# Kernel optimization log

Measured on AMD Instinct MI355X. Metric: run time of the kernel, lower is better.

Reference implementation:

```python
import jax, jax.numpy as jnp
import numpy as np

F = 26          # field_size
D = 16          # embed_dim
B = 16384       # batch
VOCABS = [1000] * F
OFFSETS = np.concatenate([[0], np.cumsum(VOCABS)[:-1]]).astype(np.int32)
IU, JU = np.triu_indices(F, k=1)   # 325 pairs (i<j)
P = IU.shape[0]
BN_EPS = 1e-3   # Keras BatchNormalization default epsilon


def setup_inputs() -> dict:
    key = jax.random.key(0)
    ks = jax.random.split(key, 8)
    s = 0.05  # keras 'random_normal' initializer stddev
    return {
        "x": jax.random.randint(ks[0], (B, F), 0, 1000, dtype=jnp.int32),
        "emb_table": jax.random.normal(ks[1], (sum(VOCABS) + 1, D), jnp.float32) * s,
        "se_w1": jax.random.normal(ks[2], (F, F // 2), jnp.float32) * s,
        "se_w2": jax.random.normal(ks[3], (F // 2, F), jnp.float32) * s,
        "bl_w": jax.random.normal(ks[4], (P, D, D), jnp.float32) * s,
        "w1": jax.random.normal(ks[5], (F * (F - 1) * D, 64), jnp.float32) * s,
        "b1": jnp.zeros((64,), jnp.float32),
        "g1": jnp.ones((64,), jnp.float32),
        "be1": jnp.zeros((64,), jnp.float32),
        "m1": jnp.zeros((64,), jnp.float32),
        "v1": jnp.ones((64,), jnp.float32),
        "w2": jax.random.normal(ks[6], (64, 32), jnp.float32) * s,
        "b2": jnp.zeros((32,), jnp.float32),
        "g2": jnp.ones((32,), jnp.float32),
        "be2": jnp.zeros((32,), jnp.float32),
        "m2": jnp.zeros((32,), jnp.float32),
        "v2": jnp.ones((32,), jnp.float32),
        "w3": jax.random.normal(ks[7], (32, 1), jnp.float32) * s,
        "b3": jnp.zeros((1,), jnp.float32),
    }


def _bilinear(v, bl_w):
    # v: [B, F, D]; shared W stack over the 325 ordered pairs (i<j)
    # tmp[p] = (v_i @ W_p) * v_j  -> [B, P, D]
    return jnp.einsum('bpd,pde->bpe', v[:, IU], bl_w) * v[:, JU]


def _bn(h, g, b, m, v):
    return g * (h - m) * jax.lax.rsqrt(v + BN_EPS) + b


def reference(x, emb_table, se_w1, se_w2, bl_w,
              w1, b1, g1, be1, m1, v1,
              w2, b2, g2, be2, m2, v2,
              w3, b3):
    ids = x + jnp.asarray(OFFSETS)
    e = emb_table[ids]                         # [B, F, D]
    # SE layer: mean-pool over embed dim, two ReLU dense layers, rescale
    z = e.mean(axis=-1)                        # [B, F]
    A = jax.nn.relu(jax.nn.relu(z @ se_w1) @ se_w2)
    se = e * A[..., None]                      # [B, F, D]
    # Bilinear interaction (same weights for both calls)
    p = _bilinear(e, bl_w).reshape(e.shape[0], -1)     # [B, P*D]
    se_p = _bilinear(se, bl_w).reshape(e.shape[0], -1)
    h = jnp.concatenate([p, se_p], axis=-1)    # [B, F*(F-1)*D]
    # MLP with inference-mode BatchNorm; dropout=0 is a no-op
    h = jax.nn.relu(_bn(h @ w1 + b1, g1, be1, m1, v1))
    h = jax.nn.relu(_bn(h @ w2 + b2, g2, be2, m2, v2))
    return jax.nn.sigmoid(h @ w3 + b3)         # [B, 1]
```

## Files before the change

### kernel.cpp

```cpp
#include <hip/hip_runtime.h>
#include <cstdint>
#include <cstddef>


#define F_FIELDS 26
#define P_PAIRS 325
#define PAD_PAIRS 336
#define BATCH 16384
#define BN_EPS 1e-3f

typedef short bf16x8 __attribute__((ext_vector_type(8)));
typedef float f32x4 __attribute__((ext_vector_type(4)));

struct PairTab { unsigned char iu[PAD_PAIRS]; unsigned char ju[PAD_PAIRS]; };
static constexpr PairTab make_pairs() {
    PairTab t{};
    int p = 0;
    for (int a = 0; a < F_FIELDS; ++a)
        for (int b = a + 1; b < F_FIELDS; ++b) { t.iu[p] = (unsigned char)a; t.ju[p] = (unsigned char)b; ++p; }
    for (; p < PAD_PAIRS; ++p) { t.iu[p] = 0; t.ju[p] = 0; }
    return t;
}
__constant__ PairTab PT = make_pairs();

__device__ __forceinline__ unsigned short bf16u(float v) {
    unsigned u = __float_as_uint(v);
    unsigned r = (u + 0x7fffu + ((u >> 16) & 1u)) >> 16;
    return (unsigned short)r;
}
__device__ __forceinline__ unsigned pk_bf16(float lo, float hi) {
    return (unsigned)bf16u(lo) | ((unsigned)bf16u(hi) << 16);
}
__device__ __forceinline__ float bflo(unsigned d) { return __uint_as_float(d << 16); }
__device__ __forceinline__ float bfhi(unsigned d) { return __uint_as_float(d & 0xffff0000u); }
__device__ __forceinline__ unsigned pk_trunc(float u, float cu) {
    return __builtin_amdgcn_perm(__float_as_uint(cu), __float_as_uint(u), 0x07060302u);
}

__global__ __launch_bounds__(256) void k_wprep(const float* __restrict__ w1,
        const float* __restrict__ blw, unsigned short* __restrict__ w1catL,
        unsigned short* __restrict__ wcatL) {
    const int p = blockIdx.x;
    const int tid = threadIdx.x;
    if (p >= P_PAIRS) {
        int4 z = make_int4(0, 0, 0, 0);
        *(int4*)(w1catL + (size_t)p * 2048 + tid * 8) = z;
        if (tid < 64) *(int4*)(wcatL + (size_t)p * 512 + tid * 8) = z;
        return;
    }
    __shared__ float wu[1024], wv[1024], wb[256];
    ((float4*)wu)[tid] = ((const float4*)(w1 + (size_t)p * 1024))[tid];
    ((float4*)wv)[tid] = ((const float4*)(w1 + 332800 + (size_t)p * 1024))[tid];
    if (tid < 64) ((float4*)wb)[tid] = ((const float4*)(blw + (size_t)p * 256))[tid];
    __syncthreads();
    {
        int nt = tid >> 6, lane = tid & 63, ln = lane & 15, q = lane >> 4;
        int o = nt * 16 + ln;
        unsigned short outv[8];
        #pragma unroll
        for (int j = 0; j < 8; ++j) {
            int k = q * 8 + j, d = k >> 1, su = k & 1;
            outv[j] = bf16u(su ? wv[d * 64 + o] : wu[d * 64 + o]);
        }
        *(int4*)(w1catL + (size_t)p * 2048 + tid * 8) = *(const int4*)outv;
    }
    if (tid < 64) {
        int ln = tid & 15, q = tid >> 4;
        unsigned short outv[8];
        #pragma unroll
        for (int j = 0; j < 8; ++j) {
            int din = q * 8 + j;
            outv[j] = (din < 16) ? bf16u(wb[din * 16 + ln]) : (unsigned short)0;
        }
        *(int4*)(wcatL + (size_t)p * 512 + tid * 8) = *(const int4*)outv;
    }
}

union __align__(16) SMem {
    struct {
        unsigned short eS[32 * 424];
        float aS[F_FIELDS * 32];
    } a;
    struct {
        unsigned ysh[8 * 4 * 64 * 4];
        float h1s[32 * 65];
        float h2s[32 * 36];
    } b;
};

__global__ __launch_bounds__(512, 4) void k_main(const int* __restrict__ x,
        const float* __restrict__ emb, const float* __restrict__ sw1,
        const float* __restrict__ sw2, const unsigned short* __restrict__ w1catL,
        const unsigned short* __restrict__ wcatL,
        const float* __restrict__ b1, const float* __restrict__ g1,
        const float* __restrict__ be1, const float* __restrict__ m1,
        const float* __restrict__ v1,
        const float* __restrict__ w2, const float* __restrict__ b2,
        const float* __restrict__ g2, const float* __restrict__ be2,
        const float* __restrict__ m2, const float* __restrict__ v2,
        const float* __restrict__ w3, const float* __restrict__ b3,
        float* __restrict__ out) {
    __shared__ SMem sm;
    __shared__ float z_s[32][F_FIELDS];
    __shared__ float sw1_s[F_FIELDS * 13];
    __shared__ float sw2_s[13 * F_FIELDS];
    const int tid = threadIdx.x;
    const int b0 = blockIdx.x * 32;
    unsigned short* eS = sm.a.eS;
    float* aS = sm.a.aS;

    for (int i = tid; i < F_FIELDS * 13; i += 512) { sw1_s[i] = sw1[i]; sw2_s[i] = sw2[i]; }
    for (int idx = tid; idx < 32 * F_FIELDS; idx += 512) {
        int r = idx / F_FIELDS, f = idx - r * F_FIELDS;
        int id = x[(b0 + r) * F_FIELDS + f] + f * 1000;
        const float4* src = (const float4*)(emb + (size_t)id * 16);
        float4 v0 = src[0], v1l = src[1], v2l = src[2], v3l = src[3];
        int4 o0, o1;
        o0.x = (int)pk_bf16(v0.x, v0.y);  o0.y = (int)pk_bf16(v0.z, v0.w);
        o0.z = (int)pk_bf16(v1l.x, v1l.y); o0.w = (int)pk_bf16(v1l.z, v1l.w);
        o1.x = (int)pk_bf16(v2l.x, v2l.y); o1.y = (int)pk_bf16(v2l.z, v2l.w);
        o1.z = (int)pk_bf16(v3l.x, v3l.y); o1.w = (int)pk_bf16(v3l.z, v3l.w);
        *(int4*)(eS + r * 424 + f * 16) = o0;
        *(int4*)(eS + r * 424 + f * 16 + 8) = o1;
        float s = v0.x + v0.y + v0.z + v0.w + v1l.x + v1l.y + v1l.z + v1l.w
                + v2l.x + v2l.y + v2l.z + v2l.w + v3l.x + v3l.y + v3l.z + v3l.w;
        z_s[r][f] = s * (1.0f / 16.0f);
    }
    __syncthreads();
    if (tid < 32) {
        float s1[13];
        #pragma unroll
        for (int o = 0; o < 13; ++o) {
            float acc0 = 0.f;
            #pragma unroll
            for (int f = 0; f < F_FIELDS; ++f) acc0 = fmaf(z_s[tid][f], sw1_s[f * 13 + o], acc0);
            s1[o] = fmaxf(acc0, 0.0f);
        }
        #pragma unroll
        for (int f = 0; f < F_FIELDS; ++f) {
            float acc0 = 0.f;
            #pragma unroll
            for (int o = 0; o < 13; ++o) acc0 = fmaf(s1[o], sw2_s[o * F_FIELDS + f], acc0);
            aS[f * 32 + tid] = fmaxf(acc0, 0.0f);
        }
    }
    __syncthreads();

    const int w    = tid >> 6;
    const int lane = tid & 63;
    const int ln   = lane & 15;
    const int q    = lane >> 4;
    const int p0 = w * 42, p1 = p0 + 42;

    f32x4 acc[2][4];
    #pragma unroll
    for (int a = 0; a < 2; ++a)
        #pragma unroll
        for (int b = 0; b < 4; ++b) acc[a][b] = (f32x4){0.f, 0.f, 0.f, 0.f};
    const f32x4 zero4 = {0.f, 0.f, 0.f, 0.f};

    bf16x8 wa[2];
    bf16x8 wb[2][4];
    #pragma unroll
    for (int s = 0; s < 2; ++s) {
        int pp = p0 + s;
        wa[s] = __builtin_bit_cast(bf16x8, *(const int4*)(wcatL + (size_t)pp * 512 + lane * 8));
        #pragma unroll
        for (int nt = 0; nt < 4; ++nt)
            wb[s][nt] = __builtin_bit_cast(bf16x8, *(const int4*)(w1catL + (size_t)pp * 2048 + nt * 512 + lane * 8));
    }

    int iu_c = PT.iu[p0];
    bf16x8 eiB[2];
    float ai[2];
    #pragma unroll
    for (int mt = 0; mt < 2; ++mt) {
        eiB[mt] = __builtin_bit_cast(bf16x8,
            *(const int4*)(eS + (mt * 16 + ln) * 424 + iu_c * 16 + (q & 1) * 8));
        ai[mt] = aS[iu_c * 32 + mt * 16 + ln];
    }

    #pragma unroll 2
    for (int p = p0; p < p1; ++p) {
        const int slot = (p - p0) & 1;
        const int ju = PT.ju[p];
        uint2 ejv[2];
        float cv[2];
        #pragma unroll
        for (int mt = 0; mt < 2; ++mt) {
            ejv[mt] = *(const uint2*)(eS + (mt * 16 + ln) * 424 + ju * 16 + q * 4);
            cv[mt]  = ai[mt] * aS[ju * 32 + mt * 16 + ln];
        }
        #pragma unroll
        for (int mt = 0; mt < 2; ++mt) {
            f32x4 t = __builtin_amdgcn_mfma_f32_16x16x32_bf16(wa[slot], eiB[mt], zero4, 0, 0, 0);
            float e0 = bflo(ejv[mt].x), e1 = bfhi(ejv[mt].x);
            float e2 = bflo(ejv[mt].y), e3 = bfhi(ejv[mt].y);
            float c  = cv[mt];
            float u0 = t[0] * e0, u1 = t[1] * e1, u2 = t[2] * e2, u3 = t[3] * e3;
            int4 af;
            af.x = (int)pk_trunc(u0, c * u0);
            af.y = (int)pk_trunc(u1, c * u1);
            af.z = (int)pk_trunc(u2, c * u2);
            af.w = (int)pk_trunc(u3, c * u3);
            bf16x8 A = __builtin_bit_cast(bf16x8, af);
            #pragma unroll
            for (int nt = 0; nt < 4; ++nt)
                acc[mt][nt] = __builtin_amdgcn_mfma_f32_16x16x32_bf16(A, wb[slot][nt], acc[mt][nt], 0, 0, 0);
        }
        {
            const int pf = (p + 2 < p1) ? (p + 2) : (p1 - 1);
            wa[slot] = __builtin_bit_cast(bf16x8, *(const int4*)(wcatL + (size_t)pf * 512 + lane * 8));
            #pragma unroll
            for (int nt = 0; nt < 4; ++nt)
                wb[slot][nt] = __builtin_bit_cast(bf16x8, *(const int4*)(w1catL + (size_t)pf * 2048 + nt * 512 + lane * 8));
        }
        const int pn = (p + 1 < p1) ? (p + 1) : p;
        const int iu_n = PT.iu[pn];
        if (iu_n != iu_c) {
            iu_c = iu_n;
            #pragma unroll
            for (int mt = 0; mt < 2; ++mt) {
                eiB[mt] = __builtin_bit_cast(bf16x8,
                    *(const int4*)(eS + (mt * 16 + ln) * 424 + iu_c * 16 + (q & 1) * 8));
                ai[mt] = aS[iu_c * 32 + mt * 16 + ln];
            }
        }
    }

    __syncthreads();
    unsigned* ysh = sm.b.ysh;
    float* h1s = sm.b.h1s;
    float* h2s = sm.b.h2s;
    #pragma unroll
    for (int mt = 0; mt < 2; ++mt)
        #pragma unroll
        for (int nh = 0; nh < 2; ++nh) {
            int nt0 = nh * 2, nt1 = nh * 2 + 1;
            int4 v;
            v.x = (int)pk_bf16(acc[mt][nt0][0], acc[mt][nt0][1]);
            v.y = (int)pk_bf16(acc[mt][nt0][2], acc[mt][nt0][3]);
            v.z = (int)pk_bf16(acc[mt][nt1][0], acc[mt][nt1][1]);
            v.w = (int)pk_bf16(acc[mt][nt1][2], acc[mt][nt1][3]);
            *(int4*)(ysh + ((w * 4 + mt * 2 + nh) * 64 + lane) * 4) = v;
        }
    __syncthreads();

    if (tid < 256) {
        const int s = tid >> 6, lane2 = tid & 63, ln2 = lane2 & 15, q2 = lane2 >> 4;
        const int mt = s >> 1, nh = s & 1;
        const int c0 = nh * 32 + ln2, c1 = c0 + 16;
        const float sc0 = g1[c0] * rsqrtf(v1[c0] + BN_EPS);
        const float of0 = be1[c0] + sc0 * (b1[c0] - m1[c0]);
        const float sc1 = g1[c1] * rsqrtf(v1[c1] + BN_EPS);
        const float of1 = be1[c1] + sc1 * (b1[c1] - m1[c1]);
        float s8[8];
        #pragma unroll
        for (int i = 0; i < 8; ++i) s8[i] = 0.f;
        #pragma unroll
        for (int wv = 0; wv < 8; ++wv) {
            int4 v = *(const int4*)(ysh + ((wv * 4 + s) * 64 + lane2) * 4);
            s8[0] += bflo((unsigned)v.x); s8[1] += bfhi((unsigned)v.x);
            s8[2] += bflo((unsigned)v.y); s8[3] += bfhi((unsigned)v.y);
            s8[4] += bflo((unsigned)v.z); s8[5] += bfhi((unsigned)v.z);
            s8[6] += bflo((unsigned)v.w); s8[7] += bfhi((unsigned)v.w);
        }
        const int row0 = mt * 16 + q2 * 4;
        #pragma unroll
        for (int r = 0; r < 4; ++r) {
            h1s[(row0 + r) * 65 + c0] = fmaxf(s8[r] * sc0 + of0, 0.f);
            h1s[(row0 + r) * 65 + c1] = fmaxf(s8[4 + r] * sc1 + of1, 0.f);
        }
    }
    __syncthreads();

    {
        const int row = tid >> 4, gg = tid & 15;
        const int o0 = gg * 2, o1 = o0 + 1;
        float a0 = 0.f, a1 = 0.f;
        #pragma unroll 8
        for (int k = 0; k < 64; ++k) {
            float hk = h1s[row * 65 + k];
            float2 wv = *(const float2*)(w2 + k * 32 + o0);
            a0 = fmaf(hk, wv.x, a0);
            a1 = fmaf(hk, wv.y, a1);
        }
        float val0 = g2[o0] * (a0 + b2[o0] - m2[o0]) * rsqrtf(v2[o0] + BN_EPS) + be2[o0];
        float val1 = g2[o1] * (a1 + b2[o1] - m2[o1]) * rsqrtf(v2[o1] + BN_EPS) + be2[o1];
        h2s[row * 36 + o0] = fmaxf(val0, 0.f);
        h2s[row * 36 + o1] = fmaxf(val1, 0.f);
    }
    __syncthreads();
    if (tid < 32) {
        float sacc = b3[0];
        #pragma unroll
        for (int k = 0; k < 32; ++k) sacc = fmaf(h2s[tid * 36 + k], w3[k], sacc);
        out[b0 + tid] = 1.0f / (1.0f + expf(-sacc));
    }
}

extern "C" void kernel_launch(void* const* d_in, const int* in_sizes, int n_in,
                              void* d_out, int out_size, void* d_ws, size_t ws_size,
                              hipStream_t stream) {
    const int*   x   = (const int*)d_in[0];
    const float* emb = (const float*)d_in[1];
    const float* sw1 = (const float*)d_in[2];
    const float* sw2 = (const float*)d_in[3];
    const float* blw = (const float*)d_in[4];
    const float* w1  = (const float*)d_in[5];
    const float* b1  = (const float*)d_in[6];
    const float* g1  = (const float*)d_in[7];
    const float* be1 = (const float*)d_in[8];
    const float* m1  = (const float*)d_in[9];
    const float* v1  = (const float*)d_in[10];
    const float* w2  = (const float*)d_in[11];
    const float* b2  = (const float*)d_in[12];
    const float* g2  = (const float*)d_in[13];
    const float* be2 = (const float*)d_in[14];
    const float* m2  = (const float*)d_in[15];
    const float* v2  = (const float*)d_in[16];
    const float* w3  = (const float*)d_in[17];
    const float* b3  = (const float*)d_in[18];
    float* out = (float*)d_out;

    char* ws = (char*)d_ws;
    unsigned short* w1catL = (unsigned short*)ws;
    unsigned short* wcatL  = (unsigned short*)(ws + 1376256);

    hipLaunchKernelGGL(k_wprep, dim3(PAD_PAIRS), dim3(256), 0, stream, w1, blw, w1catL, wcatL);
    hipLaunchKernelGGL(k_main,  dim3(512), dim3(512), 0, stream,
                       x, emb, sw1, sw2, w1catL, wcatL,
                       b1, g1, be1, m1, v1, w2, b2, g2, be2, m2, v2, w3, b3, out);
}
```

Before: 148.4 us.

## Double batch tile to 64 rows with 1024-thread blocks splitting output columns

Each block now processes 64 batch rows with 16 waves. Pairs of waves share a pair-range and split the 64 output columns, so each wave loads half the W1 fragments but reuses them over four row tiles. The goal is to halve per-row global weight traffic, at the cost of twice-recomputed first-stage bilinear MFMAs per wave pair. The first-layer reduction now runs in two passes over shared memory with extra barriers. The SE mean is recomputed from the bf16 shared copy instead of fp32 sums, which slightly changes precision. The grid drops to 256 blocks, so fewer workgroups are spread across the CUs.

```diff
diff --git a/kernel.cpp b/kernel.cpp
--- a/kernel.cpp
+++ b/kernel.cpp
@@ -78,17 +78,17 @@
 
 union __align__(16) SMem {
     struct {
-        unsigned short eS[32 * 424];
-        float aS[F_FIELDS * 32];
+        unsigned short eS[64 * 424];
+        float aS[F_FIELDS * 64];
     } a;
     struct {
         unsigned ysh[8 * 4 * 64 * 4];
-        float h1s[32 * 65];
-        float h2s[32 * 36];
+        float h1s[64 * 65];
+        float h2s[64 * 36];
     } b;
 };
 
-__global__ __launch_bounds__(512, 4) void k_main(const int* __restrict__ x,
+__global__ __launch_bounds__(1024, 4) void k_main(const int* __restrict__ x,
         const float* __restrict__ emb, const float* __restrict__ sw1,
         const float* __restrict__ sw2, const unsigned short* __restrict__ w1catL,
         const unsigned short* __restrict__ wcatL,
@@ -101,16 +101,15 @@
         const float* __restrict__ w3, const float* __restrict__ b3,
         float* __restrict__ out) {
     __shared__ SMem sm;
-    __shared__ float z_s[32][F_FIELDS];
     __shared__ float sw1_s[F_FIELDS * 13];
     __shared__ float sw2_s[13 * F_FIELDS];
     const int tid = threadIdx.x;
-    const int b0 = blockIdx.x * 32;
+    const int b0 = blockIdx.x * 64;
     unsigned short* eS = sm.a.eS;
     float* aS = sm.a.aS;
 
-    for (int i = tid; i < F_FIELDS * 13; i += 512) { sw1_s[i] = sw1[i]; sw2_s[i] = sw2[i]; }
-    for (int idx = tid; idx < 32 * F_FIELDS; idx += 512) {
+    for (int i = tid; i < F_FIELDS * 13; i += 1024) { sw1_s[i] = sw1[i]; sw2_s[i] = sw2[i]; }
+    for (int idx = tid; idx < 64 * F_FIELDS; idx += 1024) {
         int r = idx / F_FIELDS, f = idx - r * F_FIELDS;
         int id = x[(b0 + r) * F_FIELDS + f] + f * 1000;
         const float4* src = (const float4*)(emb + (size_t)id * 16);
@@ -122,18 +121,30 @@
         o1.z = (int)pk_bf16(v3l.x, v3l.y); o1.w = (int)pk_bf16(v3l.z, v3l.w);
         *(int4*)(eS + r * 424 + f * 16) = o0;
         *(int4*)(eS + r * 424 + f * 16 + 8) = o1;
-        float s = v0.x + v0.y + v0.z + v0.w + v1l.x + v1l.y + v1l.z + v1l.w
-                + v2l.x + v2l.y + v2l.z + v2l.w + v3l.x + v3l.y + v3l.z + v3l.w;
-        z_s[r][f] = s * (1.0f / 16.0f);
-    }
-    __syncthreads();
-    if (tid < 32) {
+    }
+    __syncthreads();
+    if (tid < 64) {
+        float z[F_FIELDS];
+        #pragma unroll
+        for (int f = 0; f < F_FIELDS; ++f) {
+            const int4* e16 = (const int4*)(eS + tid * 424 + f * 16);
+            int4 va = e16[0], vb = e16[1];
+            float s = bflo((unsigned)va.x) + bfhi((unsigned)va.x)
+                    + bflo((unsigned)va.y) + bfhi((unsigned)va.y)
+                    + bflo((unsigned)va.z) + bfhi((unsigned)va.z)
+                    + bflo((unsigned)va.w) + bfhi((unsigned)va.w)
+                    + bflo((unsigned)vb.x) + bfhi((unsigned)vb.x)
+                    + bflo((unsigned)vb.y) + bfhi((unsigned)vb.y)
+                    + bflo((unsigned)vb.z) + bfhi((unsigned)vb.z)
+                    + bflo((unsigned)vb.w) + bfhi((unsigned)vb.w);
+            z[f] = s * (1.0f / 16.0f);
+        }
         float s1[13];
         #pragma unroll
         for (int o = 0; o < 13; ++o) {
             float acc0 = 0.f;
             #pragma unroll
-            for (int f = 0; f < F_FIELDS; ++f) acc0 = fmaf(z_s[tid][f], sw1_s[f * 13 + o], acc0);
+            for (int f = 0; f < F_FIELDS; ++f) acc0 = fmaf(z[f], sw1_s[f * 13 + o], acc0);
             s1[o] = fmaxf(acc0, 0.0f);
         }
         #pragma unroll
@@ -141,7 +152,7 @@
             float acc0 = 0.f;
             #pragma unroll
             for (int o = 0; o < 13; ++o) acc0 = fmaf(s1[o], sw2_s[o * F_FIELDS + f], acc0);
-            aS[f * 32 + tid] = fmaxf(acc0, 0.0f);
+            aS[f * 64 + tid] = fmaxf(acc0, 0.0f);
         }
     }
     __syncthreads();
@@ -150,80 +161,83 @@
     const int lane = tid & 63;
     const int ln   = lane & 15;
     const int q    = lane >> 4;
-    const int p0 = w * 42, p1 = p0 + 42;
-
-    f32x4 acc[2][4];
+    const int c    = w >> 1;
+    const int nh   = w & 1;
+    const int p0 = c * 42, p1 = p0 + 42;
+
+    f32x4 acc[4][2];
     #pragma unroll
-    for (int a = 0; a < 2; ++a)
-        #pragma unroll
-        for (int b = 0; b < 4; ++b) acc[a][b] = (f32x4){0.f, 0.f, 0.f, 0.f};
+    for (int a = 0; a < 4; ++a)
+        #pragma unroll
+        for (int b = 0; b < 2; ++b) acc[a][b] = (f32x4){0.f, 0.f, 0.f, 0.f};
     const f32x4 zero4 = {0.f, 0.f, 0.f, 0.f};
 
     bf16x8 wa[2];
-    bf16x8 wb[2][4];
+    bf16x8 wb[2][2];
     #pragma unroll
     for (int s = 0; s < 2; ++s) {
         int pp = p0 + s;
         wa[s] = __builtin_bit_cast(bf16x8, *(const int4*)(wcatL + (size_t)pp * 512 + lane * 8));
         #pragma unroll
-        for (int nt = 0; nt < 4; ++nt)
-            wb[s][nt] = __builtin_bit_cast(bf16x8, *(const int4*)(w1catL + (size_t)pp * 2048 + nt * 512 + lane * 8));
+        for (int ntl = 0; ntl < 2; ++ntl)
+            wb[s][ntl] = __builtin_bit_cast(bf16x8,
+                *(const int4*)(w1catL + (size_t)pp * 2048 + (nh * 2 + ntl) * 512 + lane * 8));
     }
 
     int iu_c = PT.iu[p0];
-    bf16x8 eiB[2];
-    float ai[2];
+    bf16x8 eiB[4];
+    float ai[4];
     #pragma unroll
-    for (int mt = 0; mt < 2; ++mt) {
+    for (int mt = 0; mt < 4; ++mt) {
         eiB[mt] = __builtin_bit_cast(bf16x8,
             *(const int4*)(eS + (mt * 16 + ln) * 424 + iu_c * 16 + (q & 1) * 8));
-        ai[mt] = aS[iu_c * 32 + mt * 16 + ln];
+        ai[mt] = aS[iu_c * 64 + mt * 16 + ln];
     }
 
     #pragma unroll 2
     for (int p = p0; p < p1; ++p) {
         const int slot = (p - p0) & 1;
         const int ju = PT.ju[p];
-        uint2 ejv[2];
-        float cv[2];
-        #pragma unroll
-        for (int mt = 0; mt < 2; ++mt) {
+        uint2 ejv[4];
+        float cv[4];
+        #pragma unroll
+        for (int mt = 0; mt < 4; ++mt) {
             ejv[mt] = *(const uint2*)(eS + (mt * 16 + ln) * 424 + ju * 16 + q * 4);
-            cv[mt]  = ai[mt] * aS[ju * 32 + mt * 16 + ln];
-        }
-        #pragma unroll
-        for (int mt = 0; mt < 2; ++mt) {
+            cv[mt]  = ai[mt] * aS[ju * 64 + mt * 16 + ln];
+        }
+        #pragma unroll
+        for (int mt = 0; mt < 4; ++mt) {
             f32x4 t = __builtin_amdgcn_mfma_f32_16x16x32_bf16(wa[slot], eiB[mt], zero4, 0, 0, 0);
             float e0 = bflo(ejv[mt].x), e1 = bfhi(ejv[mt].x);
             float e2 = bflo(ejv[mt].y), e3 = bfhi(ejv[mt].y);
-            float c  = cv[mt];
+            float cc = cv[mt];
             float u0 = t[0] * e0, u1 = t[1] * e1, u2 = t[2] * e2, u3 = t[3] * e3;
             int4 af;
-            af.x = (int)pk_trunc(u0, c * u0);
-            af.y = (int)pk_trunc(u1, c * u1);
-            af.z = (int)pk_trunc(u2, c * u2);
-            af.w = (int)pk_trunc(u3, c * u3);
+            af.x = (int)pk_trunc(u0, cc * u0);
+            af.y = (int)pk_trunc(u1, cc * u1);
+            af.z = (int)pk_trunc(u2, cc * u2);
+            af.w = (int)pk_trunc(u3, cc * u3);
             bf16x8 A = __builtin_bit_cast(bf16x8, af);
-            #pragma unroll
-            for (int nt = 0; nt < 4; ++nt)
-                acc[mt][nt] = __builtin_amdgcn_mfma_f32_16x16x32_bf16(A, wb[slot][nt], acc[mt][nt], 0, 0, 0);
+            acc[mt][0] = __builtin_amdgcn_mfma_f32_16x16x32_bf16(A, wb[slot][0], acc[mt][0], 0, 0, 0);
+            acc[mt][1] = __builtin_amdgcn_mfma_f32_16x16x32_bf16(A, wb[slot][1], acc[mt][1], 0, 0, 0);
         }
         {
             const int pf = (p + 2 < p1) ? (p + 2) : (p1 - 1);
             wa[slot] = __builtin_bit_cast(bf16x8, *(const int4*)(wcatL + (size_t)pf * 512 + lane * 8));
             #pragma unroll
-            for (int nt = 0; nt < 4; ++nt)
-                wb[slot][nt] = __builtin_bit_cast(bf16x8, *(const int4*)(w1catL + (size_t)pf * 2048 + nt * 512 + lane * 8));
+            for (int ntl = 0; ntl < 2; ++ntl)
+                wb[slot][ntl] = __builtin_bit_cast(bf16x8,
+                    *(const int4*)(w1catL + (size_t)pf * 2048 + (nh * 2 + ntl) * 512 + lane * 8));
         }
         const int pn = (p + 1 < p1) ? (p + 1) : p;
         const int iu_n = PT.iu[pn];
         if (iu_n != iu_c) {
             iu_c = iu_n;
             #pragma unroll
-            for (int mt = 0; mt < 2; ++mt) {
+            for (int mt = 0; mt < 4; ++mt) {
                 eiB[mt] = __builtin_bit_cast(bf16x8,
                     *(const int4*)(eS + (mt * 16 + ln) * 424 + iu_c * 16 + (q & 1) * 8));
-                ai[mt] = aS[iu_c * 32 + mt * 16 + ln];
+                ai[mt] = aS[iu_c * 64 + mt * 16 + ln];
             }
         }
     }
@@ -232,47 +246,48 @@
     unsigned* ysh = sm.b.ysh;
     float* h1s = sm.b.h1s;
     float* h2s = sm.b.h2s;
+
     #pragma unroll
-    for (int mt = 0; mt < 2; ++mt)
-        #pragma unroll
-        for (int nh = 0; nh < 2; ++nh) {
-            int nt0 = nh * 2, nt1 = nh * 2 + 1;
-            int4 v;
-            v.x = (int)pk_bf16(acc[mt][nt0][0], acc[mt][nt0][1]);
-            v.y = (int)pk_bf16(acc[mt][nt0][2], acc[mt][nt0][3]);
-            v.z = (int)pk_bf16(acc[mt][nt1][0], acc[mt][nt1][1]);
-            v.w = (int)pk_bf16(acc[mt][nt1][2], acc[mt][nt1][3]);
-            *(int4*)(ysh + ((w * 4 + mt * 2 + nh) * 64 + lane) * 4) = v;
-        }
-    __syncthreads();
-
-    if (tid < 256) {
-        const int s = tid >> 6, lane2 = tid & 63, ln2 = lane2 & 15, q2 = lane2 >> 4;
-        const int mt = s >> 1, nh = s & 1;
-        const int c0 = nh * 32 + ln2, c1 = c0 + 16;
-        const float sc0 = g1[c0] * rsqrtf(v1[c0] + BN_EPS);
-        const float of0 = be1[c0] + sc0 * (b1[c0] - m1[c0]);
-        const float sc1 = g1[c1] * rsqrtf(v1[c1] + BN_EPS);
-        const float of1 = be1[c1] + sc1 * (b1[c1] - m1[c1]);
-        float s8[8];
-        #pragma unroll
-        for (int i = 0; i < 8; ++i) s8[i] = 0.f;
-        #pragma unroll
-        for (int wv = 0; wv < 8; ++wv) {
-            int4 v = *(const int4*)(ysh + ((wv * 4 + s) * 64 + lane2) * 4);
-            s8[0] += bflo((unsigned)v.x); s8[1] += bfhi((unsigned)v.x);
-            s8[2] += bflo((unsigned)v.y); s8[3] += bfhi((unsigned)v.y);
-            s8[4] += bflo((unsigned)v.z); s8[5] += bfhi((unsigned)v.z);
-            s8[6] += bflo((unsigned)v.w); s8[7] += bfhi((unsigned)v.w);
-        }
-        const int row0 = mt * 16 + q2 * 4;
-        #pragma unroll
-        for (int r = 0; r < 4; ++r) {
-            h1s[(row0 + r) * 65 + c0] = fmaxf(s8[r] * sc0 + of0, 0.f);
-            h1s[(row0 + r) * 65 + c1] = fmaxf(s8[4 + r] * sc1 + of1, 0.f);
-        }
-    }
-    __syncthreads();
+    for (int pass = 0; pass < 2; ++pass) {
+        if (nh == pass) {
+            #pragma unroll
+            for (int mt = 0; mt < 4; ++mt) {
+                int4 v;
+                v.x = (int)pk_bf16(acc[mt][0][0], acc[mt][0][1]);
+                v.y = (int)pk_bf16(acc[mt][0][2], acc[mt][0][3]);
+                v.z = (int)pk_bf16(acc[mt][1][0], acc[mt][1][1]);
+                v.w = (int)pk_bf16(acc[mt][1][2], acc[mt][1][3]);
+                *(int4*)(ysh + ((c * 4 + mt) * 64 + lane) * 4) = v;
+            }
+        }
+        __syncthreads();
+        if (tid < 256) {
+            const int mt = tid >> 6, lane2 = tid & 63, ln2 = lane2 & 15, q2 = lane2 >> 4;
+            const int c0 = pass * 32 + ln2, c1 = c0 + 16;
+            const float sc0 = g1[c0] * rsqrtf(v1[c0] + BN_EPS);
+            const float of0 = be1[c0] + sc0 * (b1[c0] - m1[c0]);
+            const float sc1 = g1[c1] * rsqrtf(v1[c1] + BN_EPS);
+            const float of1 = be1[c1] + sc1 * (b1[c1] - m1[c1]);
+            float s8[8];
+            #pragma unroll
+            for (int i = 0; i < 8; ++i) s8[i] = 0.f;
+            #pragma unroll
+            for (int cc = 0; cc < 8; ++cc) {
+                int4 v = *(const int4*)(ysh + ((cc * 4 + mt) * 64 + lane2) * 4);
+                s8[0] += bflo((unsigned)v.x); s8[1] += bfhi((unsigned)v.x);
+                s8[2] += bflo((unsigned)v.y); s8[3] += bfhi((unsigned)v.y);
+                s8[4] += bflo((unsigned)v.z); s8[5] += bfhi((unsigned)v.z);
+                s8[6] += bflo((unsigned)v.w); s8[7] += bfhi((unsigned)v.w);
+            }
+            const int row0 = mt * 16 + q2 * 4;
+            #pragma unroll
+            for (int r = 0; r < 4; ++r) {
+                h1s[(row0 + r) * 65 + c0] = fmaxf(s8[r] * sc0 + of0, 0.f);
+                h1s[(row0 + r) * 65 + c1] = fmaxf(s8[4 + r] * sc1 + of1, 0.f);
+            }
+        }
+        __syncthreads();
+    }
 
     {
         const int row = tid >> 4, gg = tid & 15;
@@ -291,7 +306,7 @@
         h2s[row * 36 + o1] = fmaxf(val1, 0.f);
     }
     __syncthreads();
-    if (tid < 32) {
+    if (tid < 64) {
         float sacc = b3[0];
         #pragma unroll
         for (int k = 0; k < 32; ++k) sacc = fmaf(h2s[tid * 36 + k], w3[k], sacc);
@@ -328,7 +343,7 @@
     unsigned short* wcatL  = (unsigned short*)(ws + 1376256);
 
     hipLaunchKernelGGL(k_wprep, dim3(PAD_PAIRS), dim3(256), 0, stream, w1, blw, w1catL, wcatL);
-    hipLaunchKernelGGL(k_main,  dim3(512), dim3(512), 0, stream,
+    hipLaunchKernelGGL(k_main,  dim3(256), dim3(1024), 0, stream,
                        x, emb, sw1, sw2, w1catL, wcatL,
                        b1, g1, be1, m1, v1, w2, b2, g2, be2, m2, v2, w3, b3, out);
 }
```

Measured after the change: 158.4 us. +6.8%, slower.
